# Performance work log

Measured on AMD Instinct MI355X. Metric: run time of the kernel, lower is better.

## Reference

```python
import jax, jax.numpy as jnp
import numpy as np

T, S, F, A, POS = 32, 4096, 256, 64, 128


def setup_inputs() -> dict:
    key = jax.random.key(0)
    ks = jax.random.split(key, 12)
    sc = lambda fan_in: 1.0 / np.sqrt(fan_in)
    return {
        "batch_data": jax.random.normal(ks[0], (T * S, F), dtype=jnp.float32),
        "xywh": jax.random.uniform(ks[1], (T * S, 4), dtype=jnp.float32),
        # nn.Linear params (y = x @ W.T + b)
        "Wa": jax.random.uniform(ks[2], (A, F), minval=-sc(F), maxval=sc(F)),
        "ba": jax.random.uniform(ks[3], (A,), minval=-sc(F), maxval=sc(F)),
        "Wb": jax.random.uniform(ks[4], (A, F), minval=-sc(F), maxval=sc(F)),
        "bb": jax.random.uniform(ks[5], (A,), minval=-sc(F), maxval=sc(F)),
        "Wg": jax.random.uniform(ks[6], (F, F), minval=-sc(F), maxval=sc(F)),
        "bg": jax.random.uniform(ks[7], (F,), minval=-sc(F), maxval=sc(F)),
        "Wh": jax.random.uniform(ks[8], (POS, 2), minval=-sc(2), maxval=sc(2)),
        "bh": jax.random.uniform(ks[9], (POS,), minval=-sc(2), maxval=sc(2)),
    }


def reference(batch_data, xywh, Wa, ba, Wb, bb, Wg, bg, Wh, bh):
    x = batch_data.reshape(T, S, F)
    pos = xywh.reshape(T, S, -1)
    # positional embedding path (computed in original forward but unused in output)
    avg_pos = jnp.mean(pos, axis=0)            # [S, 4]
    rel_pos = pos[:, :, :2] - avg_pos[:, :2]   # [T, S, 2]
    _pos_embeds = rel_pos @ Wh.T + bh          # [T, S, POS] (dead, matches source)

    theta = x @ Wa.T + ba                      # [T, S, A]
    phi = x @ Wb.T + bb                        # [T, S, A]
    feats = x @ Wg.T + bg                      # [T, S, F]

    # per-object temporal attention: attn[s, t, u] = theta[t, s] . phi[u, s]
    attn = jnp.einsum('tsa,usa->stu', theta, phi)       # [S, T, T]
    out = jnp.einsum('stu,usf->tsf', attn, feats)       # [T, S, F]
    return out
```

## Files before the change

### kernel.cpp

```cpp
#include <hip/hip_runtime.h>

#define T_ 32
#define S_ 4096
#define F_ 256
#define A_ 64
#define NS 2
#define GRID 256
#define ITERS (S_ / NS / GRID)

typedef __attribute__((ext_vector_type(8))) short s8v;
typedef __attribute__((ext_vector_type(4))) float f4v;
typedef __attribute__((ext_vector_type(4))) short s4v;

#define MFMA(a, b, c) __builtin_amdgcn_mfma_f32_16x16x32_bf16((a), (b), (c), 0, 0, 0)

__device__ __forceinline__ unsigned short f2bf(float f) {
    unsigned int u = __builtin_bit_cast(unsigned int, f);
    u += 0x7FFFu + ((u >> 16) & 1u);
    return (unsigned short)(u >> 16);
}

__global__ void convert_weights(const float* __restrict__ Wa,
                                const float* __restrict__ Wb,
                                const float* __restrict__ Wg,
                                unsigned short* __restrict__ wsB)
{
    int base = (blockIdx.x * 256 + threadIdx.x) * 4;
    const float* src;
    if (base < 16384)      src = Wa + base;
    else if (base < 32768) src = Wb + (base - 16384);
    else                   src = Wg + (base - 32768);
    float4 v = *(const float4*)src;
    s4v p;
    p[0] = (short)f2bf(v.x); p[1] = (short)f2bf(v.y);
    p[2] = (short)f2bf(v.z); p[3] = (short)f2bf(v.w);
    *(s4v*)(wsB + base) = p;
}

#define X0_OFF 0
#define X1_OFF 32768
#define WW_OFF 65536
#define TH_OFF 131072
#define PH_OFF 139264
#define AT_OFF 147456
#define FT_OFF TH_OFF
#define LDS_BYTES 151552

#define BAR() do {                                            \
    asm volatile("s_waitcnt lgkmcnt(0)" ::: "memory");        \
    __builtin_amdgcn_s_barrier();                             \
    __builtin_amdgcn_sched_barrier(0);                        \
} while (0)

__global__ __launch_bounds__(256, 1) void fused_temporal(
    const float* __restrict__ X,
    const unsigned short* __restrict__ wsB,
    const float* __restrict__ ba, const float* __restrict__ bb,
    const float* __restrict__ bg,
    float* __restrict__ out)
{
    __shared__ alignas(16) unsigned char smem[LDS_BYTES];
    const int tid  = threadIdx.x;
    const int wave = tid >> 6;
    const int lane = tid & 63;
    const int quad = lane >> 4;
    const int l15  = lane & 15;
    const int b    = blockIdx.x;

    const unsigned short* WgB = wsB + 32768;

    #pragma unroll
    for (int i = 0; i < 16; ++i) {
        int cid = i * 256 + tid;
        int r = cid >> 5, c = cid & 31;
        s8v v = *(const s8v*)(wsB + (size_t)cid * 8);
        *(s8v*)(&smem[WW_OFF + r * 512 + (((c + r) & 31) << 4)]) = v;
    }
    s8v wg[4][8];
    #pragma unroll
    for (int g = 0; g < 4; ++g) {
        const unsigned short* p = WgB + (size_t)(64 * wave + 16 * g + l15) * F_ + quad * 8;
        #pragma unroll
        for (int ks = 0; ks < 8; ++ks) wg[g][ks] = *(const s8v*)(p + ks * 32);
    }
    {
        int s0 = b * NS;
        #pragma unroll
        for (int i = 0; i < 8; ++i) {
            int linear = i * 256 + tid;
            int r = linear >> 5, c = linear & 31;
            int t = r & 31, sl = r >> 5;
            const float* xp = X + ((size_t)(t * S_ + s0 + sl)) * F_ + c * 8;
            float4 v0 = *(const float4*)(xp);
            float4 v1 = *(const float4*)(xp + 4);
            s8v p;
            p[0] = (short)f2bf(v0.x); p[1] = (short)f2bf(v0.y);
            p[2] = (short)f2bf(v0.z); p[3] = (short)f2bf(v0.w);
            p[4] = (short)f2bf(v1.x); p[5] = (short)f2bf(v1.y);
            p[6] = (short)f2bf(v1.z); p[7] = (short)f2bf(v1.w);
            *(s8v*)(&smem[X0_OFF + r * 512 + (((c + r) & 31) << 4)]) = p;
        }
    }
    float biasa = ba[16 * wave + l15];
    float biasb = bb[16 * wave + l15];
    BAR();

    float4 xnx[16];
    #pragma unroll 1
    for (int it = 0; it < ITERS; ++it) {
        const int xs = (it & 1) ? X1_OFF : X0_OFF;
        const int xd = (it & 1) ? X0_OFF : X1_OFF;
        const int s0 = (it * GRID + b) * NS;

        if (it + 1 < ITERS) {
            int sn = ((it + 1) * GRID + b) * NS;
            #pragma unroll
            for (int i = 0; i < 8; ++i) {
                int linear = i * 256 + tid;
                int r = linear >> 5, c = linear & 31;
                int t = r & 31, sl = r >> 5;
                const float* xp = X + ((size_t)(t * S_ + sn + sl)) * F_ + c * 8;
                xnx[2 * i]     = *(const float4*)(xp);
                xnx[2 * i + 1] = *(const float4*)(xp + 4);
            }
        }

        {
            const int n0 = 16 * wave;
            const int ra = n0 + l15;
            const int rb = 64 + n0 + l15;
            f4v ta[4], pa[4];
            #pragma unroll
            for (int mt = 0; mt < 4; ++mt) { ta[mt] = f4v{0.f,0.f,0.f,0.f}; pa[mt] = f4v{0.f,0.f,0.f,0.f}; }
            #pragma unroll
            for (int ks = 0; ks < 8; ++ks) {
                int chunk = 4 * ks + quad;
                s8v bfa = *(const s8v*)(&smem[WW_OFF + ra * 512 + (((chunk + ra) & 31) << 4)]);
                s8v bfb = *(const s8v*)(&smem[WW_OFF + rb * 512 + (((chunk + rb) & 31) << 4)]);
                #pragma unroll
                for (int mt = 0; mt < 4; ++mt) {
                    int r = 16 * mt + l15;
                    s8v a = *(const s8v*)(&smem[xs + r * 512 + (((chunk + r) & 31) << 4)]);
                    ta[mt] = MFMA(a, bfa, ta[mt]);
                    pa[mt] = MFMA(a, bfb, pa[mt]);
                }
            }
            int a_col = n0 + l15;
            int chunk = a_col >> 3;
            int sub   = (a_col & 7) * 2;
            #pragma unroll
            for (int mt = 0; mt < 4; ++mt) {
                #pragma unroll
                for (int r = 0; r < 4; ++r) {
                    int row = 16 * mt + quad * 4 + r;
                    int sw  = ((chunk + row) & 7) << 4;
                    *(unsigned short*)(&smem[TH_OFF + row * 128 + sw + sub]) = f2bf(ta[mt][r] + biasa);
                    *(unsigned short*)(&smem[PH_OFF + row * 128 + sw + sub]) = f2bf(pa[mt][r] + biasb);
                }
            }
        }
        BAR();

        {
            int sl  = wave >> 1;
            int mt2 = wave & 1;
            int t2  = l15 + 16 * mt2;
            int rth = sl * 32 + t2;
            #pragma unroll
            for (int nt2 = 0; nt2 < 2; ++nt2) {
                int u2  = l15 + 16 * nt2;
                int rph = sl * 32 + u2;
                f4v acc2 = {0.f,0.f,0.f,0.f};
                #pragma unroll
                for (int ks = 0; ks < 2; ++ks) {
                    int chunk = 4 * ks + quad;
                    s8v av = *(const s8v*)(&smem[TH_OFF + rth * 128 + (((chunk + rth) & 7) << 4)]);
                    s8v bv = *(const s8v*)(&smem[PH_OFF + rph * 128 + (((chunk + rph) & 7) << 4)]);
                    acc2 = MFMA(av, bv, acc2);
                }
                int chunk = u2 >> 3;
                int sub   = (u2 & 7) * 2;
                #pragma unroll
                for (int r = 0; r < 4; ++r) {
                    int tt  = quad * 4 + r + 16 * mt2;
                    int rat = sl * 32 + tt;
                    *(unsigned short*)(&smem[AT_OFF + rat * 64 + (((chunk + rat) & 3) << 4) + sub]) = f2bf(acc2[r]);
                }
            }
        }
        BAR();

        {
            s8v battn[2][2];
            #pragma unroll
            for (int sl = 0; sl < 2; ++sl) {
                #pragma unroll
                for (int nt = 0; nt < 2; ++nt) {
                    int rat = sl * 32 + l15 + 16 * nt;
                    battn[sl][nt] = *(const s8v*)(&smem[AT_OFF + rat * 64 + (((quad + rat) & 3) << 4)]);
                }
            }
            const int ftbase = FT_OFF + wave * 2048;

            f4v fa[4][4];
            #pragma unroll
            for (int g = 0; g < 4; ++g)
                #pragma unroll
                for (int mt = 0; mt < 4; ++mt) fa[g][mt] = f4v{0.f,0.f,0.f,0.f};
            #pragma unroll
            for (int ks = 0; ks < 8; ++ks) {
                int chunk = 4 * ks + quad;
                s8v a[4];
                #pragma unroll
                for (int mt = 0; mt < 4; ++mt) {
                    int r = 16 * mt + l15;
                    a[mt] = *(const s8v*)(&smem[xs + r * 512 + (((chunk + r) & 31) << 4)]);
                }
                #pragma unroll
                for (int g = 0; g < 4; ++g)
                    #pragma unroll
                    for (int mt = 0; mt < 4; ++mt)
                        fa[g][mt] = MFMA(a[mt], wg[g][ks], fa[g][mt]);
            }

            #pragma unroll
            for (int g = 0; g < 4; ++g) {
                int n0 = 64 * wave + 16 * g;
                float biasg = bg[n0 + l15];
                #pragma unroll
                for (int mt = 0; mt < 4; ++mt) {
                    int sl = mt >> 1;
                    int u0 = (mt & 1) * 16 + quad * 4;
                    s4v pk;
                    #pragma unroll
                    for (int r = 0; r < 4; ++r) pk[r] = (short)f2bf(fa[g][mt][r] + biasg);
                    int addr = ftbase + sl * 1024 + l15 * 64 + ((((u0 >> 3) + l15) & 3) << 4) + (u0 & 7) * 2;
                    *(s4v*)(&smem[addr]) = pk;
                }
                int f0 = n0 + 4 * quad;
                #pragma unroll
                for (int sl = 0; sl < 2; ++sl) {
                    s8v avf = *(const s8v*)(&smem[ftbase + sl * 1024 + l15 * 64 + (((quad + l15) & 3) << 4)]);
                    #pragma unroll
                    for (int nt = 0; nt < 2; ++nt) {
                        f4v z = {0.f,0.f,0.f,0.f};
                        f4v acc = MFMA(avf, battn[sl][nt], z);
                        int t = l15 + 16 * nt;
                        float4 st;
                        st.x = acc[0]; st.y = acc[1]; st.z = acc[2]; st.w = acc[3];
                        *(float4*)(out + ((size_t)(t * S_ + s0 + sl)) * F_ + f0) = st;
                    }
                }
            }
        }

        if (it + 1 < ITERS) {
            #pragma unroll
            for (int i = 0; i < 8; ++i) {
                int linear = i * 256 + tid;
                int r = linear >> 5, c = linear & 31;
                float4 v0 = xnx[2 * i];
                float4 v1 = xnx[2 * i + 1];
                s8v p;
                p[0] = (short)f2bf(v0.x); p[1] = (short)f2bf(v0.y);
                p[2] = (short)f2bf(v0.z); p[3] = (short)f2bf(v0.w);
                p[4] = (short)f2bf(v1.x); p[5] = (short)f2bf(v1.y);
                p[6] = (short)f2bf(v1.z); p[7] = (short)f2bf(v1.w);
                *(s8v*)(&smem[xd + r * 512 + (((c + r) & 31) << 4)]) = p;
            }
        }
        BAR();
    }
}

extern "C" void kernel_launch(void* const* d_in, const int* in_sizes, int n_in,
                              void* d_out, int out_size, void* d_ws, size_t ws_size,
                              hipStream_t stream) {
    (void)in_sizes; (void)n_in; (void)ws_size; (void)out_size;
    const float* X  = (const float*)d_in[0];
    const float* Wa = (const float*)d_in[2];
    const float* ba = (const float*)d_in[3];
    const float* Wb = (const float*)d_in[4];
    const float* bb = (const float*)d_in[5];
    const float* Wg = (const float*)d_in[6];
    const float* bg = (const float*)d_in[7];
    float* out = (float*)d_out;
    unsigned short* wsB = (unsigned short*)d_ws;

    convert_weights<<<dim3(96), dim3(256), 0, stream>>>(Wa, Wb, Wg, wsB);
    fused_temporal<<<dim3(GRID), dim3(256), 0, stream>>>(X, wsB, ba, bb, bg, out);
}
```

Before: 305.0 us.

## Double waves per block and hold theta/phi weights in registers

Launches 512 threads per block instead of 256, so each block has eight waves. The Wa/Wb projection, Wg feature GEMM, attention tiles and per-wave feature staging are all split across the eight waves. The Wa/Wb weight fragments now live in per-wave registers rather than in a swizzled LDS copy, which drops those LDS reads and shrinks LDS use. The aim is more latency hiding and MFMA parallelism per CU, since the grid has only one block per CU. The cost is more block-wide barrier contention and a different register budget under the new launch bounds.

```diff
diff --git a/kernel.cpp b/kernel.cpp
--- a/kernel.cpp
+++ b/kernel.cpp
@@ -39,12 +39,11 @@
 
 #define X0_OFF 0
 #define X1_OFF 32768
-#define WW_OFF 65536
-#define TH_OFF 131072
-#define PH_OFF 139264
-#define AT_OFF 147456
-#define FT_OFF TH_OFF
-#define LDS_BYTES 151552
+#define TH_OFF 65536
+#define PH_OFF 73728
+#define AT_OFF 81920
+#define FT_OFF 86016
+#define LDS_BYTES 118784
 
 #define BAR() do {                                            \
     asm volatile("s_waitcnt lgkmcnt(0)" ::: "memory");        \
@@ -52,7 +51,7 @@
     __builtin_amdgcn_sched_barrier(0);                        \
 } while (0)
 
-__global__ __launch_bounds__(256, 1) void fused_temporal(
+__global__ __launch_bounds__(512, 2) void fused_temporal(
     const float* __restrict__ X,
     const unsigned short* __restrict__ wsB,
     const float* __restrict__ ba, const float* __restrict__ bb,
@@ -69,25 +68,29 @@
 
     const unsigned short* WgB = wsB + 32768;
 
+    s8v wabfrag[8];
+    {
+        const unsigned short* p = wsB + (wave < 4 ? 0 : 16384)
+                                + (size_t)(16 * (wave & 3) + l15) * F_ + quad * 8;
+        #pragma unroll
+        for (int ks = 0; ks < 8; ++ks) wabfrag[ks] = *(const s8v*)(p + ks * 32);
+    }
+    const float bias_ab = (wave < 4 ? ba : bb)[16 * (wave & 3) + l15];
+
+    s8v wg[2][8];
     #pragma unroll
-    for (int i = 0; i < 16; ++i) {
-        int cid = i * 256 + tid;
-        int r = cid >> 5, c = cid & 31;
-        s8v v = *(const s8v*)(wsB + (size_t)cid * 8);
-        *(s8v*)(&smem[WW_OFF + r * 512 + (((c + r) & 31) << 4)]) = v;
-    }
-    s8v wg[4][8];
-    #pragma unroll
-    for (int g = 0; g < 4; ++g) {
-        const unsigned short* p = WgB + (size_t)(64 * wave + 16 * g + l15) * F_ + quad * 8;
+    for (int g = 0; g < 2; ++g) {
+        const unsigned short* p = WgB + (size_t)(32 * wave + 16 * g + l15) * F_ + quad * 8;
         #pragma unroll
         for (int ks = 0; ks < 8; ++ks) wg[g][ks] = *(const s8v*)(p + ks * 32);
     }
+    const float biasg[2] = { bg[32 * wave + l15], bg[32 * wave + 16 + l15] };
+
     {
         int s0 = b * NS;
         #pragma unroll
-        for (int i = 0; i < 8; ++i) {
-            int linear = i * 256 + tid;
+        for (int i = 0; i < 4; ++i) {
+            int linear = i * 512 + tid;
             int r = linear >> 5, c = linear & 31;
             int t = r & 31, sl = r >> 5;
             const float* xp = X + ((size_t)(t * S_ + s0 + sl)) * F_ + c * 8;
@@ -101,11 +104,9 @@
             *(s8v*)(&smem[X0_OFF + r * 512 + (((c + r) & 31) << 4)]) = p;
         }
     }
-    float biasa = ba[16 * wave + l15];
-    float biasb = bb[16 * wave + l15];
     BAR();
 
-    float4 xnx[16];
+    float4 xnx[8];
     #pragma unroll 1
     for (int it = 0; it < ITERS; ++it) {
         const int xs = (it & 1) ? X1_OFF : X0_OFF;
@@ -115,8 +116,8 @@
         if (it + 1 < ITERS) {
             int sn = ((it + 1) * GRID + b) * NS;
             #pragma unroll
-            for (int i = 0; i < 8; ++i) {
-                int linear = i * 256 + tid;
+            for (int i = 0; i < 4; ++i) {
+                int linear = i * 512 + tid;
                 int r = linear >> 5, c = linear & 31;
                 int t = r & 31, sl = r >> 5;
                 const float* xp = X + ((size_t)(t * S_ + sn + sl)) * F_ + c * 8;
@@ -126,26 +127,21 @@
         }
 
         {
-            const int n0 = 16 * wave;
-            const int ra = n0 + l15;
-            const int rb = 64 + n0 + l15;
-            f4v ta[4], pa[4];
-            #pragma unroll
-            for (int mt = 0; mt < 4; ++mt) { ta[mt] = f4v{0.f,0.f,0.f,0.f}; pa[mt] = f4v{0.f,0.f,0.f,0.f}; }
+            f4v ac[4];
+            #pragma unroll
+            for (int mt = 0; mt < 4; ++mt) ac[mt] = f4v{0.f,0.f,0.f,0.f};
             #pragma unroll
             for (int ks = 0; ks < 8; ++ks) {
                 int chunk = 4 * ks + quad;
-                s8v bfa = *(const s8v*)(&smem[WW_OFF + ra * 512 + (((chunk + ra) & 31) << 4)]);
-                s8v bfb = *(const s8v*)(&smem[WW_OFF + rb * 512 + (((chunk + rb) & 31) << 4)]);
                 #pragma unroll
                 for (int mt = 0; mt < 4; ++mt) {
                     int r = 16 * mt + l15;
                     s8v a = *(const s8v*)(&smem[xs + r * 512 + (((chunk + r) & 31) << 4)]);
-                    ta[mt] = MFMA(a, bfa, ta[mt]);
-                    pa[mt] = MFMA(a, bfb, pa[mt]);
-                }
-            }
-            int a_col = n0 + l15;
+                    ac[mt] = MFMA(a, wabfrag[ks], ac[mt]);
+                }
+            }
+            const int dst = (wave < 4) ? TH_OFF : PH_OFF;
+            int a_col = 16 * (wave & 3) + l15;
             int chunk = a_col >> 3;
             int sub   = (a_col & 7) * 2;
             #pragma unroll
@@ -154,38 +150,35 @@
                 for (int r = 0; r < 4; ++r) {
                     int row = 16 * mt + quad * 4 + r;
                     int sw  = ((chunk + row) & 7) << 4;
-                    *(unsigned short*)(&smem[TH_OFF + row * 128 + sw + sub]) = f2bf(ta[mt][r] + biasa);
-                    *(unsigned short*)(&smem[PH_OFF + row * 128 + sw + sub]) = f2bf(pa[mt][r] + biasb);
+                    *(unsigned short*)(&smem[dst + row * 128 + sw + sub]) = f2bf(ac[mt][r] + bias_ab);
                 }
             }
         }
         BAR();
 
         {
-            int sl  = wave >> 1;
-            int mt2 = wave & 1;
+            int sl  = wave >> 2;
+            int mt2 = (wave >> 1) & 1;
+            int nt2 = wave & 1;
             int t2  = l15 + 16 * mt2;
+            int u2  = l15 + 16 * nt2;
             int rth = sl * 32 + t2;
-            #pragma unroll
-            for (int nt2 = 0; nt2 < 2; ++nt2) {
-                int u2  = l15 + 16 * nt2;
-                int rph = sl * 32 + u2;
-                f4v acc2 = {0.f,0.f,0.f,0.f};
-                #pragma unroll
-                for (int ks = 0; ks < 2; ++ks) {
-                    int chunk = 4 * ks + quad;
-                    s8v av = *(const s8v*)(&smem[TH_OFF + rth * 128 + (((chunk + rth) & 7) << 4)]);
-                    s8v bv = *(const s8v*)(&smem[PH_OFF + rph * 128 + (((chunk + rph) & 7) << 4)]);
-                    acc2 = MFMA(av, bv, acc2);
-                }
-                int chunk = u2 >> 3;
-                int sub   = (u2 & 7) * 2;
-                #pragma unroll
-                for (int r = 0; r < 4; ++r) {
-                    int tt  = quad * 4 + r + 16 * mt2;
-                    int rat = sl * 32 + tt;
-                    *(unsigned short*)(&smem[AT_OFF + rat * 64 + (((chunk + rat) & 3) << 4) + sub]) = f2bf(acc2[r]);
-                }
+            int rph = sl * 32 + u2;
+            f4v acc2 = {0.f,0.f,0.f,0.f};
+            #pragma unroll
+            for (int ks = 0; ks < 2; ++ks) {
+                int chunk = 4 * ks + quad;
+                s8v av = *(const s8v*)(&smem[TH_OFF + rth * 128 + (((chunk + rth) & 7) << 4)]);
+                s8v bv = *(const s8v*)(&smem[PH_OFF + rph * 128 + (((chunk + rph) & 7) << 4)]);
+                acc2 = MFMA(av, bv, acc2);
+            }
+            int chunk = u2 >> 3;
+            int sub   = (u2 & 7) * 2;
+            #pragma unroll
+            for (int r = 0; r < 4; ++r) {
+                int tt  = quad * 4 + r + 16 * mt2;
+                int rat = sl * 32 + tt;
+                *(unsigned short*)(&smem[AT_OFF + rat * 64 + (((chunk + rat) & 3) << 4) + sub]) = f2bf(acc2[r]);
             }
         }
         BAR();
@@ -200,47 +193,43 @@
                     battn[sl][nt] = *(const s8v*)(&smem[AT_OFF + rat * 64 + (((quad + rat) & 3) << 4)]);
                 }
             }
-            const int ftbase = FT_OFF + wave * 2048;
-
-            f4v fa[4][4];
-            #pragma unroll
-            for (int g = 0; g < 4; ++g)
+            const int ftbase = FT_OFF + wave * 4096;
+
+            f4v fa[2][4];
+            #pragma unroll
+            for (int g = 0; g < 2; ++g)
                 #pragma unroll
                 for (int mt = 0; mt < 4; ++mt) fa[g][mt] = f4v{0.f,0.f,0.f,0.f};
             #pragma unroll
             for (int ks = 0; ks < 8; ++ks) {
                 int chunk = 4 * ks + quad;
-                s8v a[4];
                 #pragma unroll
                 for (int mt = 0; mt < 4; ++mt) {
                     int r = 16 * mt + l15;
-                    a[mt] = *(const s8v*)(&smem[xs + r * 512 + (((chunk + r) & 31) << 4)]);
-                }
-                #pragma unroll
-                for (int g = 0; g < 4; ++g)
-                    #pragma unroll
-                    for (int mt = 0; mt < 4; ++mt)
-                        fa[g][mt] = MFMA(a[mt], wg[g][ks], fa[g][mt]);
-            }
-
-            #pragma unroll
-            for (int g = 0; g < 4; ++g) {
-                int n0 = 64 * wave + 16 * g;
-                float biasg = bg[n0 + l15];
+                    s8v a = *(const s8v*)(&smem[xs + r * 512 + (((chunk + r) & 31) << 4)]);
+                    fa[0][mt] = MFMA(a, wg[0][ks], fa[0][mt]);
+                    fa[1][mt] = MFMA(a, wg[1][ks], fa[1][mt]);
+                }
+            }
+
+            #pragma unroll
+            for (int g = 0; g < 2; ++g) {
+                int fl = 16 * g + l15;
                 #pragma unroll
                 for (int mt = 0; mt < 4; ++mt) {
                     int sl = mt >> 1;
                     int u0 = (mt & 1) * 16 + quad * 4;
                     s4v pk;
                     #pragma unroll
-                    for (int r = 0; r < 4; ++r) pk[r] = (short)f2bf(fa[g][mt][r] + biasg);
-                    int addr = ftbase + sl * 1024 + l15 * 64 + ((((u0 >> 3) + l15) & 3) << 4) + (u0 & 7) * 2;
+                    for (int r = 0; r < 4; ++r) pk[r] = (short)f2bf(fa[g][mt][r] + biasg[g]);
+                    int addr = ftbase + sl * 2048 + fl * 64
+                             + ((((u0 >> 3) + fl) & 3) << 4) + (u0 & 7) * 2;
                     *(s4v*)(&smem[addr]) = pk;
                 }
-                int f0 = n0 + 4 * quad;
+                int f0 = 32 * wave + 16 * g + 4 * quad;
                 #pragma unroll
                 for (int sl = 0; sl < 2; ++sl) {
-                    s8v avf = *(const s8v*)(&smem[ftbase + sl * 1024 + l15 * 64 + (((quad + l15) & 3) << 4)]);
+                    s8v avf = *(const s8v*)(&smem[ftbase + sl * 2048 + fl * 64 + (((quad + fl) & 3) << 4)]);
                     #pragma unroll
                     for (int nt = 0; nt < 2; ++nt) {
                         f4v z = {0.f,0.f,0.f,0.f};
@@ -256,8 +245,8 @@
 
         if (it + 1 < ITERS) {
             #pragma unroll
-            for (int i = 0; i < 8; ++i) {
-                int linear = i * 256 + tid;
+            for (int i = 0; i < 4; ++i) {
+                int linear = i * 512 + tid;
                 int r = linear >> 5, c = linear & 31;
                 float4 v0 = xnx[2 * i];
                 float4 v1 = xnx[2 * i + 1];
@@ -288,5 +277,5 @@
     unsigned short* wsB = (unsigned short*)d_ws;
 
     convert_weights<<<dim3(96), dim3(256), 0, stream>>>(Wa, Wb, Wg, wsB);
-    fused_temporal<<<dim3(GRID), dim3(256), 0, stream>>>(X, wsB, ba, bb, bg, out);
-}
+    fused_temporal<<<dim3(GRID), dim3(512), 0, stream>>>(X, wsB, ba, bb, bg, out);
+}
```

New measurement: 362.1 us. 18.7% more time.
